# Optimization experiments

Hardware: AMD Instinct MI355X
Metric: run time of the kernel (lower is better)

Reference implementation:

```python
import jax, jax.numpy as jnp
import numpy as np

B, D, F, K = 16384, 768, 8192, 32

def setup_inputs() -> dict:
    key = jax.random.key(0)
    k0, k1, k2 = jax.random.split(key, 3)
    x = jax.random.normal(k0, (B, D), dtype=jnp.float32)
    # encoder weight ~ orthogonal-ish scale; exact init scheme doesn't affect the math being tested
    W_enc = jax.random.normal(k1, (F, D), dtype=jnp.float32) / np.sqrt(D)
    b_enc = jnp.zeros((F,), dtype=jnp.float32)
    W_dec = jax.random.normal(k2, (D, F), dtype=jnp.float32)
    # torch init normalizes decoder.weight rows (dim=1)
    W_dec = W_dec / jnp.linalg.norm(W_dec, axis=1, keepdims=True)
    dec_bias = jnp.zeros((D,), dtype=jnp.float32)
    return {"x": x, "W_enc": W_enc, "b_enc": b_enc, "W_dec": W_dec, "dec_bias": dec_bias, "k": K}


def reference(x, W_enc, b_enc, W_dec, dec_bias, k):
    # encode: center, linear, relu
    x_centered = x - dec_bias                              # [B, D]
    acts = jax.nn.relu(jnp.einsum('bd,fd->bf', x_centered, W_enc) + b_enc)  # [B, F]
    # topk + scatter into dense sparse code
    vals, idx = jax.lax.top_k(acts, k)                     # [B, k]
    rows = jnp.arange(acts.shape[0])[:, None]              # [B, 1]
    sparse_code = jnp.zeros_like(acts).at[rows, idx].set(vals)  # [B, F]
    # decode: dense GEMM over mostly-zero code + bias
    reconstruction = jnp.einsum('bf,df->bd', sparse_code, W_dec) + dec_bias  # [B, D]
    return reconstruction, sparse_code
```

## Files before the change

kernel.cpp:

```cpp
#include <hip/hip_runtime.h>

#define NB 16384
#define ND 768
#define NF 8192
#define CMAX 512
#define SEGW 16
#define GSEG 1024
#define AMAX 128
#define MARG 0.07f
#define THETA0 2.0f
#define THETA0_BITS 0x4000u

typedef __attribute__((ext_vector_type(8))) short bf16x8;
typedef __attribute__((ext_vector_type(4))) float f32x4;
typedef __attribute__((ext_vector_type(4))) unsigned int u32x4;
typedef __attribute__((ext_vector_type(2))) float f32x2;

__device__ inline unsigned short f2bf(float f) {
  unsigned u = __float_as_uint(f);
  unsigned r = (u + 0x7FFFu + ((u >> 16) & 1u)) >> 16;
  return (unsigned short)r;
}
__device__ inline float bfbits2f(unsigned u16) { return __uint_as_float(u16 << 16); }

__global__ __launch_bounds__(256) void cvt_bf16_k(const float* __restrict__ in,
                                                  unsigned short* __restrict__ out) {
  size_t t = (size_t)blockIdx.x * 256 + threadIdx.x;
  const float4* i4 = (const float4*)in;
  float4 a = i4[t * 2], b = i4[t * 2 + 1];
  ushort4 lo = make_ushort4(f2bf(a.x), f2bf(a.y), f2bf(a.z), f2bf(a.w));
  ushort4 hi = make_ushort4(f2bf(b.x), f2bf(b.y), f2bf(b.z), f2bf(b.w));
  ((ushort4*)out)[t * 2] = lo;
  ((ushort4*)out)[t * 2 + 1] = hi;
}

__global__ __launch_bounds__(256) void beta_k(const float* __restrict__ W_enc,
                                              const float* __restrict__ b_enc,
                                              const float* __restrict__ dec_bias,
                                              float* __restrict__ beta) {
  int f = blockIdx.x * 4 + (threadIdx.x >> 6);
  int lane = threadIdx.x & 63;
  const float* wr = W_enc + (size_t)f * ND;
  float s = 0.f;
  for (int d = lane; d < ND; d += 64) s += dec_bias[d] * wr[d];
  for (int off = 32; off; off >>= 1) s += __shfl_down(s, off);
  if (lane == 0) beta[f] = b_enc[f] - s;
}

__global__ __launch_bounds__(256) void transpose_bf_k(const float* __restrict__ in,
                                                      unsigned short* __restrict__ out) {
  __shared__ float tile[32][33];
  int lx = threadIdx.x & 31;
  int ty = threadIdx.x >> 5;
  int x = blockIdx.x * 32 + lx;
  for (int j = ty; j < 32; j += 8) {
    int y = blockIdx.y * 32 + j;
    tile[j][lx] = in[(size_t)y * NF + x];
  }
  __syncthreads();
  int xo = blockIdx.y * 32 + lx;
  for (int j = ty; j < 32; j += 8) {
    int yo = blockIdx.x * 32 + j;
    out[(size_t)yo * ND + xo] = f2bf(tile[lx][j]);
  }
}

__global__ __launch_bounds__(256) void enc_gemm_bf16(
    const unsigned short* __restrict__ Xb, const unsigned short* __restrict__ Wb,
    const float* __restrict__ beta, unsigned* __restrict__ glist) {
  __shared__ __align__(1024) unsigned short As[128 * 64];
  __shared__ __align__(1024) unsigned short Bs[128 * 64];
  const int tid = threadIdx.x;
  const int wave = tid >> 6, lane = tid & 63;
  const int wm = wave >> 1, wn = wave & 1;

  const int orig = blockIdx.y * gridDim.x + blockIdx.x;
  const int xcd = orig & 7;
  const int local = orig >> 3;
  const int tcol = local >> 4;
  const int trow = (xcd << 4) + (local & 15);
  const int brow = trow << 7;
  const int bcol = tcol << 7;

  f32x4 acc[4][4] = {};

  const int srow = tid >> 3;
  const int scol = (((tid & 7) ^ ((tid >> 3) & 7)) << 3);
  const unsigned short* gA = Xb + (size_t)(brow + srow) * ND + scol;
  const unsigned short* gB = Wb + (size_t)(bcol + srow) * ND + scol;

#pragma unroll 1
  for (int step = 0; step < 12; ++step) {
    const int kt = step * 64;
#pragma unroll
    for (int i = 0; i < 4; ++i) {
      __builtin_amdgcn_global_load_lds(
          (const __attribute__((address_space(1))) void*)(gA + (size_t)(i * 32) * ND + kt),
          (__attribute__((address_space(3))) void*)(As + (i * 32 + wave * 8) * 64), 16, 0, 0);
      __builtin_amdgcn_global_load_lds(
          (const __attribute__((address_space(1))) void*)(gB + (size_t)(i * 32) * ND + kt),
          (__attribute__((address_space(3))) void*)(Bs + (i * 32 + wave * 8) * 64), 16, 0, 0);
    }
    __syncthreads();
#pragma unroll
    for (int kk = 0; kk < 64; kk += 32) {
      const int chunk = (kk + ((lane >> 4) << 3)) >> 3;
      const int rA = (wm << 6) + (lane & 15);
      const int rB = (wn << 6) + (lane & 15);
      const int sw = chunk ^ (lane & 7);
      bf16x8 a[4], bvv[4];
#pragma unroll
      for (int m = 0; m < 4; ++m)
        a[m] = *(const bf16x8*)&As[(rA + (m << 4)) * 64 + (sw << 3)];
#pragma unroll
      for (int n = 0; n < 4; ++n)
        bvv[n] = *(const bf16x8*)&Bs[(rB + (n << 4)) * 64 + (sw << 3)];
#pragma unroll
      for (int m = 0; m < 4; ++m)
#pragma unroll
        for (int n = 0; n < 4; ++n)
          acc[m][n] = __builtin_amdgcn_mfma_f32_16x16x32_bf16(a[m], bvv[n], acc[m][n], 0, 0, 0);
    }
    __syncthreads();
  }

  unsigned (*wseg)[SEGW] = (unsigned (*)[SEGW])As;
  unsigned* wcnt = (unsigned*)(As + 4096);
#pragma unroll
  for (int i = 0; i < 8; ++i) ((unsigned*)wseg)[tid + 256 * i] = 0u;
  if (tid < 128) wcnt[tid] = 0u;
  __syncthreads();

#pragma unroll
  for (int n = 0; n < 4; ++n) {
    float bet = beta[bcol + (wn << 6) + (n << 4) + (lane & 15)];
#pragma unroll
    for (int m = 0; m < 4; ++m) {
#pragma unroll
      for (int r = 0; r < 4; ++r) {
        int row_l = (wm << 6) + (m << 4) + ((lane >> 4) << 2) + r;
        int col_l = (wn << 6) + (n << 4) + (lane & 15);
        float v = fmaxf(acc[m][n][r] + bet, 0.f);
        unsigned short ub = f2bf(v);
        if (ub >= (unsigned short)THETA0_BITS) {
          unsigned p = atomicAdd(&wcnt[row_l], 1u);
          if (p < SEGW) wseg[row_l][p] = ((unsigned)ub << 16) | (unsigned)(bcol + col_l);
        }
      }
    }
  }
  __syncthreads();
  {
    int row = tid >> 1;
    int sbase = (tid & 1) << 3;
    u32x4 v0 = *(const u32x4*)&wseg[row][sbase];
    u32x4 v1 = *(const u32x4*)&wseg[row][sbase + 4];
    if (sbase == 0 && wcnt[row] > SEGW) v0[0] = 0xFFFFFFFFu;
    unsigned* dst = &glist[(size_t)(brow + row) * GSEG + (tcol << 4)];
    __builtin_nontemporal_store(v0, (u32x4*)&dst[sbase]);
    __builtin_nontemporal_store(v1, (u32x4*)&dst[sbase + 4]);
  }
}

__global__ __launch_bounds__(256, 6) void ksel_k(
    const unsigned* __restrict__ glist,
    const float* __restrict__ x, const float* __restrict__ W_enc,
    const float* __restrict__ beta, const unsigned short* __restrict__ WdecBf,
    const float* __restrict__ dec_bias, const int* __restrict__ kptr,
    float* __restrict__ out_rec, float* __restrict__ g_vals, int* __restrict__ g_idxs) {
  const int tid = threadIdx.x, wave = tid >> 6, lane = tid & 63;
  const int b = blockIdx.x * 4 + wave;
  int k = *kptr; k = k < 1 ? 1 : (k > 64 ? 64 : k);
  const unsigned kk = (unsigned)k;

  __shared__ unsigned clist_s[4][CMAX];
  __shared__ unsigned long long aval_s[4][AMAX];
  __shared__ float selv_s[4][64];
  __shared__ int seli_s[4][64];
  __shared__ int ctrC_s[4], ctrW_s[4], ctrA_s[4];
  __shared__ int blkFb;
  __shared__ float fb_x[ND];
  __shared__ unsigned long long fbl[512];
  __shared__ unsigned fb_thrmax[256];
  __shared__ unsigned long long fb_red[4];
  __shared__ unsigned fb_cnt4[4];
  __shared__ unsigned fbcnt;

  unsigned* clist = clist_s[wave];
  unsigned long long* aval = aval_s[wave];
  float* selv = selv_s[wave];
  int* seli = seli_s[wave];

  if (tid == 0) blkFb = 0;
  if (lane == 0) { ctrC_s[wave] = 0; ctrW_s[wave] = 0; ctrA_s[wave] = 0; }

  bool bad = false;
  {
    const u32x4* seg4 = (const u32x4*)(glist + (size_t)b * GSEG);
#pragma unroll
    for (int ii = 0; ii < 4; ++ii) {
      u32x4 e4 = __builtin_nontemporal_load(&seg4[lane + (ii << 6)]);
#pragma unroll
      for (int q = 0; q < 4; ++q) {
        unsigned e = e4[q];
        if (e) {
          if ((e & 0xFFFFu) >= (unsigned)NF) bad = true;
          else {
            int p = atomicAdd(&ctrC_s[wave], 1);
            if (p < CMAX) clist[p] = e;
          }
        }
      }
    }
  }
  bad = (__ballot(bad) != 0ull);
  int n = ctrC_s[wave]; if (n > CMAX) n = CMAX;

  unsigned ks[8];
#pragma unroll
  for (int ii = 0; ii < 8; ++ii) {
    int j = lane + (ii << 6);
    ks[ii] = (j < n) ? (clist[j] >> 16) : 0u;
  }
  unsigned T = 0;
  for (int bit = 14; bit >= 0; --bit) {
    unsigned probe = T | (1u << bit);
    int c = 0;
#pragma unroll
    for (int ii = 0; ii < 8; ++ii) c += (ks[ii] >= probe);
#pragma unroll
    for (int off = 32; off; off >>= 1) c += __shfl_xor(c, off);
    if (c >= (int)kk) T = probe;
  }
  float tauf = bfbits2f(T);

  bool valid = !bad && (n >= k) && (tauf >= THETA0 + MARG);
  if (lane == 0 && !valid) atomicOr(&blkFb, 1);
  __syncthreads();

  if (!blkFb) {
    const float thrW = tauf + MARG;
    const float thrA = tauf - MARG;
    for (int j = lane; j < n; j += 64) {
      unsigned e = clist[j];
      float v = bfbits2f(e >> 16);
      int idx = (int)(e & 0xFFFFu);
      if (v > thrW) {
        int p = atomicAdd(&ctrW_s[wave], 1);
        if (p < 63) { selv[p] = v; seli[p] = idx; }
      } else if (v >= thrA) {
        int p = atomicAdd(&ctrA_s[wave], 1);
        if (p < AMAX) aval[p] = (unsigned long long)(unsigned)idx;
      }
    }
    __syncthreads();
    int c = ctrW_s[wave]; if (c > 63) c = 63; if (c > k - 1) c = k - 1;
    int na = ctrA_s[wave]; if (na > AMAX) na = AMAX;

    float xr[12];
#pragma unroll
    for (int cc = 0; cc < 12; ++cc)
      xr[cc] = __builtin_nontemporal_load(&x[(size_t)b * ND + lane + 64 * cc]);
    for (int j = 0; j < na; j += 2) {
      int f0 = (int)(unsigned)aval[j];
      int f1 = (j + 1 < na) ? (int)(unsigned)aval[j + 1] : f0;
      const float* w0 = W_enc + (size_t)f0 * ND;
      const float* w1 = W_enc + (size_t)f1 * ND;
      float s0 = 0.f, s1 = 0.f;
#pragma unroll
      for (int cc = 0; cc < 12; ++cc) {
        s0 = fmaf(xr[cc], w0[lane + 64 * cc], s0);
        s1 = fmaf(xr[cc], w1[lane + 64 * cc], s1);
      }
#pragma unroll
      for (int off = 32; off; off >>= 1) {
        s0 += __shfl_xor(s0, off);
        s1 += __shfl_xor(s1, off);
      }
      if (lane == 0) {
        float v0 = fmaxf(s0 + beta[f0], 0.f);
        aval[j] = (((unsigned long long)__float_as_uint(v0)) << 13) | (unsigned)(8191 - f0);
        if (j + 1 < na) {
          float v1 = fmaxf(s1 + beta[f1], 0.f);
          aval[j + 1] = (((unsigned long long)__float_as_uint(v1)) << 13) | (unsigned)(8191 - f1);
        }
      }
    }
    __syncthreads();

    unsigned long long p0 = (lane < na) ? aval[lane] : 0ull;
    unsigned long long p1 = (lane + 64 < na) ? aval[lane + 64] : 0ull;
    int rounds = k - c; if (rounds < 0) rounds = 0;
    for (int r = 0; r < rounds; ++r) {
      unsigned long long m = p0 > p1 ? p0 : p1;
#pragma unroll
      for (int off = 32; off; off >>= 1) {
        unsigned long long o = __shfl_xor(m, off);
        if (o > m) m = o;
      }
      if (lane == 0) {
        if (m) { selv[c + r] = __uint_as_float((unsigned)(m >> 13)); seli[c + r] = 8191 - (int)(m & 0x1FFFull); }
        else   { selv[c + r] = 0.f; seli[c + r] = 0; }
      }
      if (p0 == m) p0 = 0;
      if (p1 == m) p1 = 0;
    }
    __syncthreads();
  } else {
    for (int r = 0; r < 4; ++r) {
      const int row = blockIdx.x * 4 + r;
      fb_x[tid] = x[(size_t)row * ND + tid];
      fb_x[tid + 256] = x[(size_t)row * ND + tid + 256];
      fb_x[tid + 512] = x[(size_t)row * ND + tid + 512];
      __syncthreads();
      unsigned mymax = 0u;
      for (int j = 0; j < 32; ++j) {
        int f = tid * 32 + j;
        const float* w = W_enc + (size_t)f * ND;
        float s = 0.f;
#pragma unroll 8
        for (int d = 0; d < ND; ++d) s = fmaf(fb_x[d], w[d], s);
        unsigned bits = __float_as_uint(fmaxf(s + beta[f], 0.f));
        if (bits > mymax) mymax = bits;
      }
      fb_thrmax[tid] = mymax;
      __syncthreads();
      unsigned L = 0;
      for (int bit = 30; bit >= 0; --bit) {
        unsigned probe = L | (1u << bit);
        unsigned long long bl = __ballot(fb_thrmax[tid] >= probe);
        if (lane == 0) fb_cnt4[wave] = (unsigned)__popcll(bl);
        __syncthreads();
        unsigned tot = fb_cnt4[0] + fb_cnt4[1] + fb_cnt4[2] + fb_cnt4[3];
        if (tot >= kk) L = probe;
        __syncthreads();
      }
      if (tid == 0) fbcnt = 0u;
      __syncthreads();
      for (int j = 0; j < 32; ++j) {
        int f = tid * 32 + j;
        const float* w = W_enc + (size_t)f * ND;
        float s = 0.f;
#pragma unroll 8
        for (int d = 0; d < ND; ++d) s = fmaf(fb_x[d], w[d], s);
        unsigned bits = __float_as_uint(fmaxf(s + beta[f], 0.f));
        if (bits >= L) {
          unsigned p = atomicAdd(&fbcnt, 1u);
          if (p < 512) fbl[p] = (((unsigned long long)bits) << 13) | (unsigned)(8191 - f);
        }
      }
      __syncthreads();
      int n2 = (int)(fbcnt < 512u ? fbcnt : 512u);
      for (int rr = 0; rr < k; ++rr) {
        unsigned long long best = 0ull;
        for (int j2 = tid; j2 < n2; j2 += 256)
          if (fbl[j2] > best) best = fbl[j2];
#pragma unroll
        for (int off = 32; off; off >>= 1) {
          unsigned long long o = __shfl_xor(best, off);
          if (o > best) best = o;
        }
        if (lane == 0) fb_red[wave] = best;
        __syncthreads();
        unsigned long long m = fb_red[0];
#pragma unroll
        for (int w2 = 1; w2 < 4; ++w2)
          if (fb_red[w2] > m) m = fb_red[w2];
        if (tid == 0) {
          if (m) { selv_s[r][rr] = __uint_as_float((unsigned)(m >> 13)); seli_s[r][rr] = 8191 - (int)(m & 0x1FFFull); }
          else   { selv_s[r][rr] = 0.f; seli_s[r][rr] = 0; }
        }
        for (int j2 = tid; j2 < n2; j2 += 256)
          if (fbl[j2] == m) fbl[j2] = 0ull;
        __syncthreads();
      }
      __syncthreads();
    }
  }

  if (lane < k) {
    g_vals[(size_t)b * 64 + lane] = selv[lane];
    g_idxs[(size_t)b * 64 + lane] = seli[lane];
  }

  float acc[12];
#pragma unroll
  for (int cc = 0; cc < 6; ++cc) {
    float2 db = *(const float2*)&dec_bias[cc * 128 + lane * 2];
    acc[2 * cc] = db.x; acc[2 * cc + 1] = db.y;
  }
#define RECON_TERM(r)                                                          \
  {                                                                            \
    int f = seli[r]; float v = selv[r];                                        \
    const unsigned short* wd = WdecBf + (size_t)f * ND;                        \
    _Pragma("unroll")                                                          \
    for (int cc = 0; cc < 6; ++cc) {                                           \
      unsigned pr = *(const unsigned*)&wd[cc * 128 + lane * 2];                \
      acc[2 * cc] = fmaf(v, bfbits2f(pr & 0xFFFFu), acc[2 * cc]);              \
      acc[2 * cc + 1] = fmaf(v, bfbits2f(pr >> 16), acc[2 * cc + 1]);          \
    }                                                                          \
  }
  if (k == 32) {
#pragma unroll
    for (int r = 0; r < 32; ++r) RECON_TERM(r)
  } else {
    for (int r = 0; r < k; ++r) RECON_TERM(r)
  }
#pragma unroll
  for (int cc = 0; cc < 6; ++cc) {
    f32x2 st = {acc[2 * cc], acc[2 * cc + 1]};
    __builtin_nontemporal_store(st, (f32x2*)&out_rec[(size_t)b * ND + cc * 128 + lane * 2]);
  }
}

__global__ __launch_bounds__(256) void d2_sparse_k(
    const float* __restrict__ g_vals, const int* __restrict__ g_idxs,
    const int* __restrict__ kptr, float* __restrict__ out_sc) {
  const int b = blockIdx.x, tid = threadIdx.x;
  int k = *kptr; k = k < 1 ? 1 : (k > 64 ? 64 : k);
  __shared__ float row[NF];
  __shared__ float sv[64];
  __shared__ int si[64];
  if (tid < k) { sv[tid] = g_vals[(size_t)b * 64 + tid]; si[tid] = g_idxs[(size_t)b * 64 + tid]; }
  float4* r4 = (float4*)row;
#pragma unroll
  for (int i = 0; i < 8; ++i) r4[tid + 256 * i] = make_float4(0.f, 0.f, 0.f, 0.f);
  __syncthreads();
  if (tid < k) row[si[tid]] = sv[tid];
  __syncthreads();
  f32x4* o4 = (f32x4*)(out_sc + (size_t)b * NF);
  const f32x4* r4v = (const f32x4*)row;
#pragma unroll
  for (int i = 0; i < 8; ++i)
    __builtin_nontemporal_store(r4v[tid + 256 * i], &o4[tid + 256 * i]);
}

extern "C" void kernel_launch(void* const* d_in, const int* in_sizes, int n_in,
                              void* d_out, int out_size, void* d_ws, size_t ws_size,
                              hipStream_t stream) {
  const float* x        = (const float*)d_in[0];
  const float* W_enc    = (const float*)d_in[1];
  const float* b_enc    = (const float*)d_in[2];
  const float* W_dec    = (const float*)d_in[3];
  const float* dec_bias = (const float*)d_in[4];
  const int*   kptr     = (const int*)d_in[5];

  float* out_rec = (float*)d_out;
  float* out_sc  = (float*)d_out + (size_t)NB * ND;

  char* scb = (char*)out_sc;
  unsigned*       glist = (unsigned*)scb;
  unsigned short* Xbf   = (unsigned short*)(scb + 67108864);
  unsigned short* Wbf   = (unsigned short*)(scb + 92274688);

  char* ws = (char*)d_ws;
  unsigned short* WdecBf = (unsigned short*)ws;
  float* beta   = (float*)(ws + 12582912);
  float* g_vals = (float*)(ws + 12615680);
  int*   g_idxs = (int*)(ws + 16809984);

  cvt_bf16_k<<<(NB * ND) / 2048, 256, 0, stream>>>(x, Xbf);
  cvt_bf16_k<<<(NF * ND) / 2048, 256, 0, stream>>>(W_enc, Wbf);
  beta_k<<<NF / 4, 256, 0, stream>>>(W_enc, b_enc, dec_bias, beta);
  transpose_bf_k<<<dim3(NF / 32, ND / 32), 256, 0, stream>>>(W_dec, WdecBf);
  enc_gemm_bf16<<<dim3(NF / 128, NB / 128), 256, 0, stream>>>(Xbf, Wbf, beta, glist);
  ksel_k<<<NB / 4, 256, 0, stream>>>(glist, x, W_enc, beta, WdecBf, dec_bias, kptr,
                                     out_rec, g_vals, g_idxs);
  d2_sparse_k<<<NB, 256, 0, stream>>>(g_vals, g_idxs, kptr, out_sc);
}
```

Before: 571.8 us.

## Double-buffer encoder GEMM LDS tiles with 32-wide K stages

```diff
diff --git a/kernel.cpp b/kernel.cpp
--- a/kernel.cpp
+++ b/kernel.cpp
@@ -68,8 +68,8 @@
 __global__ __launch_bounds__(256) void enc_gemm_bf16(
     const unsigned short* __restrict__ Xb, const unsigned short* __restrict__ Wb,
     const float* __restrict__ beta, unsigned* __restrict__ glist) {
-  __shared__ __align__(1024) unsigned short As[128 * 64];
-  __shared__ __align__(1024) unsigned short Bs[128 * 64];
+  __shared__ __align__(1024) unsigned short As[2][64 * 64];
+  __shared__ __align__(1024) unsigned short Bs[2][64 * 64];
   const int tid = threadIdx.x;
   const int wave = tid >> 6, lane = tid & 63;
   const int wm = wave >> 1, wn = wave & 1;
@@ -84,48 +84,77 @@
 
   f32x4 acc[4][4] = {};
 
-  const int srow = tid >> 3;
-  const int scol = (((tid & 7) ^ ((tid >> 3) & 7)) << 3);
-  const unsigned short* gA = Xb + (size_t)(brow + srow) * ND + scol;
-  const unsigned short* gB = Wb + (size_t)(bcol + srow) * ND + scol;
-
+  int row0, k20, row1, k21;
+  {
+    int cid = tid, line = cid >> 3, slot = cid & 7, v = slot ^ (line & 7);
+    row0 = 2 * line + (v >> 2); k20 = v & 3;
+  }
+  {
+    int cid = 256 + tid, line = cid >> 3, slot = cid & 7, v = slot ^ (line & 7);
+    row1 = 2 * line + (v >> 2); k21 = v & 3;
+  }
+  const unsigned short* gA0 = Xb + (size_t)(brow + row0) * ND + k20 * 8;
+  const unsigned short* gA1 = Xb + (size_t)(brow + row1) * ND + k21 * 8;
+  const unsigned short* gB0 = Wb + (size_t)(bcol + row0) * ND + k20 * 8;
+  const unsigned short* gB1 = Wb + (size_t)(bcol + row1) * ND + k21 * 8;
+
+#define STAGE(bs, kt)                                                          \
+  {                                                                            \
+    __builtin_amdgcn_global_load_lds(                                          \
+        (const __attribute__((address_space(1))) void*)(gA0 + (kt)),           \
+        (__attribute__((address_space(3))) void*)(&As[bs][wave * 512]), 16, 0, 0); \
+    __builtin_amdgcn_global_load_lds(                                          \
+        (const __attribute__((address_space(1))) void*)(gA1 + (kt)),           \
+        (__attribute__((address_space(3))) void*)(&As[bs][2048 + wave * 512]), 16, 0, 0); \
+    __builtin_amdgcn_global_load_lds(                                          \
+        (const __attribute__((address_space(1))) void*)(gB0 + (kt)),           \
+        (__attribute__((address_space(3))) void*)(&Bs[bs][wave * 512]), 16, 0, 0); \
+    __builtin_amdgcn_global_load_lds(                                          \
+        (const __attribute__((address_space(1))) void*)(gB1 + (kt)),           \
+        (__attribute__((address_space(3))) void*)(&Bs[bs][2048 + wave * 512]), 16, 0, 0); \
+  }
+
+#define COMPUTE(bs)                                                            \
+  {                                                                            \
+    const int K2 = lane >> 4;                                                  \
+    const int rA = (wm << 6) + (lane & 15);                                    \
+    const int rB = (wn << 6) + (lane & 15);                                    \
+    bf16x8 a[4], bvv[4];                                                       \
+    _Pragma("unroll")                                                          \
+    for (int m = 0; m < 4; ++m) {                                              \
+      int r = rA + (m << 4);                                                   \
+      int line = r >> 1;                                                       \
+      int slot = (((r & 1) << 2) + K2) ^ (line & 7);                           \
+      a[m] = *(const bf16x8*)&As[bs][line * 64 + slot * 8];                    \
+    }                                                                          \
+    _Pragma("unroll")                                                          \
+    for (int n = 0; n < 4; ++n) {                                              \
+      int r = rB + (n << 4);                                                   \
+      int line = r >> 1;                                                       \
+      int slot = (((r & 1) << 2) + K2) ^ (line & 7);                           \
+      bvv[n] = *(const bf16x8*)&Bs[bs][line * 64 + slot * 8];                  \
+    }                                                                          \
+    _Pragma("unroll")                                                          \
+    for (int m = 0; m < 4; ++m)                                                \
+      _Pragma("unroll")                                                        \
+      for (int n = 0; n < 4; ++n)                                              \
+        acc[m][n] = __builtin_amdgcn_mfma_f32_16x16x32_bf16(a[m], bvv[n], acc[m][n], 0, 0, 0); \
+  }
+
+  STAGE(0, 0)
+  __syncthreads();
 #pragma unroll 1
-  for (int step = 0; step < 12; ++step) {
-    const int kt = step * 64;
-#pragma unroll
-    for (int i = 0; i < 4; ++i) {
-      __builtin_amdgcn_global_load_lds(
-          (const __attribute__((address_space(1))) void*)(gA + (size_t)(i * 32) * ND + kt),
-          (__attribute__((address_space(3))) void*)(As + (i * 32 + wave * 8) * 64), 16, 0, 0);
-      __builtin_amdgcn_global_load_lds(
-          (const __attribute__((address_space(1))) void*)(gB + (size_t)(i * 32) * ND + kt),
-          (__attribute__((address_space(3))) void*)(Bs + (i * 32 + wave * 8) * 64), 16, 0, 0);
-    }
+  for (int it = 0; it < 12; ++it) {
+    STAGE(1, (2 * it + 1) * 32)
+    COMPUTE(0)
     __syncthreads();
-#pragma unroll
-    for (int kk = 0; kk < 64; kk += 32) {
-      const int chunk = (kk + ((lane >> 4) << 3)) >> 3;
-      const int rA = (wm << 6) + (lane & 15);
-      const int rB = (wn << 6) + (lane & 15);
-      const int sw = chunk ^ (lane & 7);
-      bf16x8 a[4], bvv[4];
-#pragma unroll
-      for (int m = 0; m < 4; ++m)
-        a[m] = *(const bf16x8*)&As[(rA + (m << 4)) * 64 + (sw << 3)];
-#pragma unroll
-      for (int n = 0; n < 4; ++n)
-        bvv[n] = *(const bf16x8*)&Bs[(rB + (n << 4)) * 64 + (sw << 3)];
-#pragma unroll
-      for (int m = 0; m < 4; ++m)
-#pragma unroll
-        for (int n = 0; n < 4; ++n)
-          acc[m][n] = __builtin_amdgcn_mfma_f32_16x16x32_bf16(a[m], bvv[n], acc[m][n], 0, 0, 0);
-    }
+    if (it < 11) STAGE(0, (2 * it + 2) * 32)
+    COMPUTE(1)
     __syncthreads();
   }
 
   unsigned (*wseg)[SEGW] = (unsigned (*)[SEGW])As;
-  unsigned* wcnt = (unsigned*)(As + 4096);
+  unsigned* wcnt = (unsigned*)((unsigned short*)As + 4096);
 #pragma unroll
   for (int i = 0; i < 8; ++i) ((unsigned*)wseg)[tid + 256 * i] = 0u;
   if (tid < 128) wcnt[tid] = 0u;
```

Result: slower. 609.4 us (+6.6%).
